# Performance work log

Measured on AMD Instinct MI355X. Metric: run time of the kernel, lower is better.

Reference implementation:

```python
import jax, jax.numpy as jnp
import numpy as np

B, C, HH, WW = 256, 1024, 7, 7
S = HH * WW            # 49 tokens
D = 1024               # hidden_size
L = 2                  # encoder_layers (nhead arg, swapped in source)
H = 2                  # attention heads (num_layers arg, swapped in source)
HD = D // H            # 512 head dim
FF = 1024              # encoder_ffn_dim
OUT = 1024             # head output
EPS = 1e-5


def setup_inputs() -> dict:
    key = jax.random.key(0)
    ks = jax.random.split(key, 10)
    n = lambda k, shape: jax.random.normal(k, shape, jnp.float32) * 0.02
    return dict(
        x=jax.random.normal(ks[0], (B, C, HH, WW), jnp.float32),
        pos_emb=n(ks[1], (S, D)),
        ln1_s=jnp.ones((L, D), jnp.float32), ln1_b=jnp.zeros((L, D), jnp.float32),
        wq=n(ks[2], (L, D, D)), wk=n(ks[3], (L, D, D)),
        wv=n(ks[4], (L, D, D)), wo=n(ks[5], (L, D, D)),
        ln2_s=jnp.ones((L, D), jnp.float32), ln2_b=jnp.zeros((L, D), jnp.float32),
        w1=n(ks[6], (L, D, FF)), b1=jnp.zeros((L, FF), jnp.float32),
        w2=n(ks[7], (L, FF, D)), b2=jnp.zeros((L, D), jnp.float32),
        lnf_s=jnp.ones((D,), jnp.float32), lnf_b=jnp.zeros((D,), jnp.float32),
        head_w=n(ks[8], (S * D, OUT)), head_b=jnp.zeros((OUT,), jnp.float32),
    )


def _ln(x, s, b):
    m = jnp.mean(x, axis=-1, keepdims=True)
    v = jnp.var(x, axis=-1, keepdims=True)
    return (x - m) * jax.lax.rsqrt(v + EPS) * s + b


def reference(x, pos_emb, ln1_s, ln1_b, wq, wk, wv, wo, ln2_s, ln2_b,
              w1, b1, w2, b2, lnf_s, lnf_b, head_w, head_b):
    b = x.shape[0]
    # flatten HxW then permute -> [B, S, D] token sequence
    h = x.reshape(b, C, S).transpose(0, 2, 1)
    # BigBirdPegasus encoder: learned pos emb added to inputs_embeds (no scaling path)
    h = h + pos_emb[None, :, :]
    scale = 1.0 / jnp.sqrt(jnp.float32(HD))
    for i in range(L):
        # --- self-attention block (pre-LN); seq_len=49 triggers original_full attention ---
        r = h
        hn = _ln(h, ln1_s[i], ln1_b[i])
        q = (hn @ wq[i]).reshape(b, S, H, HD)
        k = (hn @ wk[i]).reshape(b, S, H, HD)
        v = (hn @ wv[i]).reshape(b, S, H, HD)
        scores = jnp.einsum('bqhd,bkhd->bhqk', q, k) * scale
        attn = jax.nn.softmax(scores, axis=-1)
        ctx = jnp.einsum('bhqk,bkhd->bqhd', attn, v).reshape(b, S, D)
        h = r + ctx @ wo[i]
        # --- feed-forward block (pre-LN, gelu_new) ---
        r = h
        hn = _ln(h, ln2_s[i], ln2_b[i])
        hn = jax.nn.gelu(hn @ w1[i] + b1[i], approximate=True)
        h = r + hn @ w2[i] + b2[i]
    # BigBirdPegasus applies layernorm_embedding AFTER the layer stack
    h = _ln(h, lnf_s, lnf_b)
    # flatten + linear + relu head
    out = jax.nn.relu(h.reshape(b, S * D) @ head_w + head_b)
    return out
```

## Files before the change

kernel.cpp:

```cpp
#include <hip/hip_runtime.h>
#include <hip/hip_bf16.h>
#include <stdint.h>

#define Bq 256
#define Sq 49
#define Dq 1024
#define Hq 2
#define HDq 512
#define Mq (Bq*Sq)
#define KHEADq (Sq*Dq)
#define STq 3072

typedef unsigned short u16;
typedef short bf16x8 __attribute__((ext_vector_type(8)));
typedef float f32x4 __attribute__((ext_vector_type(4)));

__device__ inline u16 f2bf(float f){
  union { float f; uint32_t u; } c; c.f = f;
  uint32_t r = c.u + 0x7FFFu + ((c.u >> 16) & 1u);
  return (u16)(r >> 16);
}

#define GLOAD_LDS16(gp, lp) \
  __builtin_amdgcn_global_load_lds((__attribute__((address_space(1))) void*)(gp), \
                                   (__attribute__((address_space(3))) void*)(lp), 16, 0, 0)
#define MFMA16(a,b,c) __builtin_amdgcn_mfma_f32_16x16x32_bf16(a,b,c,0,0,0)

__global__ __launch_bounds__(256) void prep_kernel(const float* __restrict__ x,
    const float* __restrict__ pos, float* __restrict__ h){
  __shared__ float t[49*129];
  int b = blockIdx.x, c0 = blockIdx.y*128;
  int tid = threadIdx.x, lane = tid & 63, wave = tid >> 6;
  const float* xb = x + (size_t)b*(Dq*Sq) + (size_t)c0*Sq;
  #pragma unroll
  for(int i=0;i<32;i++){
    int cc = wave + i*4;
    if(lane < Sq) t[lane*129 + cc] = xb[(size_t)cc*Sq + lane];
  }
  __syncthreads();
  #pragma unroll
  for(int p=0;p<25;p++){
    int idx = p*256 + tid;
    int s = idx >> 7, cc = idx & 127;
    if(s < Sq)
      h[((size_t)b*Sq + s)*Dq + c0 + cc] = t[s*129 + cc] + pos[s*Dq + c0 + cc];
  }
}

__global__ __launch_bounds__(256) void ln_kernel(const float* __restrict__ hin,
    const float* __restrict__ sc, const float* __restrict__ bi, u16* __restrict__ outp){
  int wave = threadIdx.x >> 6, lane = threadIdx.x & 63;
  int row = blockIdx.x*4 + wave;
  const float* p = hin + (size_t)row*Dq + lane*16;
  float v[16];
  #pragma unroll
  for(int i=0;i<4;i++){
    f32x4 t = *(const f32x4*)(p + i*4);
    v[4*i]=t[0]; v[4*i+1]=t[1]; v[4*i+2]=t[2]; v[4*i+3]=t[3];
  }
  float s=0.f, sq=0.f;
  #pragma unroll
  for(int i=0;i<16;i++){ s += v[i]; sq += v[i]*v[i]; }
  #pragma unroll
  for(int o=32;o>=1;o>>=1){ s += __shfl_xor(s,o); sq += __shfl_xor(sq,o); }
  float mean = s * (1.f/Dq);
  float var  = sq * (1.f/Dq) - mean*mean;
  float rs = rsqrtf(var + 1e-5f);
  int c0 = lane*16;
  uint32_t w[8];
  #pragma unroll
  for(int i=0;i<8;i++){
    u16 lo = f2bf((v[2*i]   - mean)*rs*sc[c0+2*i]   + bi[c0+2*i]);
    u16 hi = f2bf((v[2*i+1] - mean)*rs*sc[c0+2*i+1] + bi[c0+2*i+1]);
    w[i] = (uint32_t)lo | ((uint32_t)hi << 16);
  }
  uint4* ob = (uint4*)(outp + (size_t)row*Dq + c0);
  ob[0] = make_uint4(w[0],w[1],w[2],w[3]);
  ob[1] = make_uint4(w[4],w[5],w[6],w[7]);
}

__global__ void transp_all(const float* __restrict__ wq, const float* __restrict__ wk,
    const float* __restrict__ wv, const float* __restrict__ wo,
    const float* __restrict__ w1, const float* __restrict__ w2, u16* __restrict__ outp){
  __shared__ float t[32][33];
  int slot = blockIdx.z; int l = slot / 6, j = slot - l*6;
  const float* srcs[6] = {wq,wk,wv,wo,w1,w2};
  const float* in = srcs[j] + (size_t)l*Dq*Dq;
  u16* o = outp + (size_t)slot*Dq*Dq;
  int k0 = blockIdx.x*32, n0 = blockIdx.y*32;
  int tx = threadIdx.x, ty = threadIdx.y;
  #pragma unroll
  for(int i=0;i<4;i++) t[ty+8*i][tx] = in[(size_t)(k0+ty+8*i)*Dq + n0+tx];
  __syncthreads();
  #pragma unroll
  for(int i=0;i<4;i++) o[(size_t)(n0+ty+8*i)*Dq + k0+tx] = f2bf(t[tx][ty+8*i]);
}

template<int EPI>
__global__ __launch_bounds__(512, 2) void gemm_nt2(
    const u16* __restrict__ A, int lda,
    const u16* __restrict__ Bt, int ldb,
    void* __restrict__ Cout, const float* __restrict__ resid,
    const float* __restrict__ bias, int ldc)
{
  __shared__ u16 lds[65536];
  int tid = threadIdx.x, lane = tid & 63;
  int wave = tid >> 6;
  int wm = wave >> 2, wn = wave & 3;
  int l15 = lane & 15, l4 = lane >> 4;
  int swz = (l15 & 7) << 4;

  int gx = gridDim.x, nwg = gx*gridDim.y;
  int orig = blockIdx.y*gx + blockIdx.x;
  int qq = nwg >> 3, rr = nwg & 7;
  int xcd = orig & 7, idx = orig >> 3;
  int wgid = (xcd < rr ? xcd*(qq+1) : rr*(qq+1) + (xcd-rr)*qq) + idx;
  int bx = wgid % gx, by = wgid / gx;
  int m0 = by*256, n0 = bx*256;

  int srow = tid >> 3, scolb = (tid & 7) * 16;
  int scolx = scolb ^ ((srow & 7) << 4);
  auto stage2 = [&](int d, int kt, int h){
    #pragma unroll
    for(int cc=0; cc<2; cc++){
      int c = 2*h + cc;
      if(c < 4){
        int row = c*64 + srow;
        const u16* src = A + (size_t)(m0+row)*lda + kt*64 + (scolx>>1);
        GLOAD_LDS16(src, &lds[d*16384 + c*4096 + tid*8]);
      } else {
        int c4 = c - 4;
        int row = c4*64 + srow;
        const u16* src = Bt + (size_t)(n0+row)*ldb + kt*64 + (scolx>>1);
        GLOAD_LDS16(src, &lds[32768 + d*16384 + c4*4096 + tid*8]);
      }
    }
  };
  auto rdA = [&](int d, int i, int s)->bf16x8{
    int row = wm*128 + i*16 + l15;
    int byt = row*128 + ((s*64 + l4*16) ^ swz);
    return *(const bf16x8*)((const char*)lds + d*32768 + byt);
  };
  auto rdB = [&](int d, int n, int s)->bf16x8{
    int row = wn*64 + n*16 + l15;
    int byt = row*128 + ((s*64 + l4*16) ^ swz);
    return *(const bf16x8*)((const char*)lds + 65536 + d*32768 + byt);
  };

  f32x4 acc[8][4] = {};
  bf16x8 bfr[4][2];

  #pragma unroll
  for(int h=0;h<4;h++) stage2(0, 0, h);

  for(int t=0; t<16; ++t){
    int d = t & 1;
    if(t+1 < 16){
      stage2(d^1, t+1, 0);
      asm volatile("s_waitcnt vmcnt(2)" ::: "memory");
    } else {
      asm volatile("s_waitcnt vmcnt(0)" ::: "memory");
    }
    __builtin_amdgcn_sched_barrier(0);
    __builtin_amdgcn_s_barrier();
    #pragma unroll
    for(int n=0;n<4;n++)
      #pragma unroll
      for(int s=0;s<2;s++)
        bfr[n][s] = rdB(d, n, s);
    {
      bf16x8 a00 = rdA(d,0,0), a01 = rdA(d,0,1), a10 = rdA(d,1,0), a11 = rdA(d,1,1);
      __builtin_amdgcn_s_setprio(1);
      #pragma unroll
      for(int n=0;n<4;n++){
        acc[0][n] = MFMA16(a00, bfr[n][0], acc[0][n]);
        acc[0][n] = MFMA16(a01, bfr[n][1], acc[0][n]);
        acc[1][n] = MFMA16(a10, bfr[n][0], acc[1][n]);
        acc[1][n] = MFMA16(a11, bfr[n][1], acc[1][n]);
      }
      __builtin_amdgcn_s_setprio(0);
      __builtin_amdgcn_s_barrier();
    }
    #pragma unroll
    for(int q=1;q<4;q++){
      bf16x8 a00 = rdA(d,2*q,0), a01 = rdA(d,2*q,1), a10 = rdA(d,2*q+1,0), a11 = rdA(d,2*q+1,1);
      if(t+1 < 16) stage2(d^1, t+1, q);
      __builtin_amdgcn_s_barrier();
      __builtin_amdgcn_s_setprio(1);
      #pragma unroll
      for(int n=0;n<4;n++){
        acc[2*q][n]   = MFMA16(a00, bfr[n][0], acc[2*q][n]);
        acc[2*q][n]   = MFMA16(a01, bfr[n][1], acc[2*q][n]);
        acc[2*q+1][n] = MFMA16(a10, bfr[n][0], acc[2*q+1][n]);
        acc[2*q+1][n] = MFMA16(a11, bfr[n][1], acc[2*q+1][n]);
      }
      __builtin_amdgcn_s_setprio(0);
      __builtin_amdgcn_s_barrier();
    }
  }

  if constexpr (EPI == 1){
    float* slot = (float*)((char*)lds + wave*4096);
    float bv[4];
    #pragma unroll
    for(int n=0;n<4;n++) bv[n] = bias ? bias[n0 + wn*64 + n*16 + l15] : 0.f;
    #pragma unroll
    for(int i=0;i<8;i++){
      #pragma unroll
      for(int n=0;n<4;n++)
        #pragma unroll
        for(int r=0;r<4;r++)
          slot[(l4*4+r)*64 + n*16 + l15] = acc[i][n][r] + bv[n];
      #pragma unroll
      for(int st=0;st<4;st++){
        int u = st*64 + lane;
        int row = u >> 4, c4 = (u & 15)*4;
        f32x4 v4 = *(const f32x4*)&slot[row*64 + c4];
        size_t o = (size_t)(m0 + wm*128 + i*16 + row)*ldc + n0 + wn*64 + c4;
        f32x4 r4 = *(const f32x4*)&resid[o];
        *(f32x4*)((float*)Cout + o) = v4 + r4;
      }
    }
  } else {
    u16* slot = (u16*)((char*)lds + wave*2048);
    float bv[4];
    if constexpr (EPI == 2){
      #pragma unroll
      for(int n=0;n<4;n++) bv[n] = bias[n0 + wn*64 + n*16 + l15];
    }
    #pragma unroll
    for(int i=0;i<8;i++){
      #pragma unroll
      for(int n=0;n<4;n++)
        #pragma unroll
        for(int r=0;r<4;r++){
          float va = acc[i][n][r];
          u16 ov;
          if constexpr (EPI == 0){
            ov = f2bf(va);
          } else {
            float xg = va + bv[n];
            float tg = tanhf(0.79788456080286536f*(xg + 0.044715f*xg*xg*xg));
            ov = f2bf(0.5f*xg*(1.f+tg));
          }
          slot[(l4*4+r)*64 + n*16 + l15] = ov;
        }
      #pragma unroll
      for(int st=0;st<2;st++){
        int u = st*64 + lane;
        int row = u >> 3, c8 = (u & 7)*8;
        bf16x8 v8 = *(const bf16x8*)&slot[row*64 + c8];
        *(bf16x8*)((u16*)Cout + (size_t)(m0 + wm*128 + i*16 + row)*ldc + n0 + wn*64 + c8) = v8;
      }
    }
  }
}

__global__ __launch_bounds__(256) void gemm_head(
    const u16* __restrict__ A, const float* __restrict__ W,
    float* __restrict__ parts)
{
  __shared__ u16 sA[128*32];
  __shared__ float sC[4][1024];
  int tid = threadIdx.x, lane = tid & 63;
  int wave = tid >> 6;
  int wm = wave >> 1, wn = wave & 1;
  int l15 = lane & 15, l4 = lane >> 4;
  int nwg = gridDim.x*gridDim.y*gridDim.z;
  int orig = (blockIdx.z*gridDim.y + blockIdx.y)*gridDim.x + blockIdx.x;
  int cpx = nwg >> 3;
  int swz = (orig & 7)*cpx + (orig >> 3);
  int bx = swz & 7, by = (swz >> 3) & 1, z = swz >> 4;
  int m0 = by*128, n0 = bx*128;
  size_t abase = (size_t)m0*KHEADq + (size_t)z*1024;
  f32x4 acc[4][4] = {};
  const float* wp = W + ((size_t)z*1024 + (size_t)l4*8)*1024 + n0 + wn*64 + l15;
  for(int kt=0;kt<32;kt++){
    #pragma unroll
    for(int c=0;c<2;c++){
      int s2 = c*256+tid;
      GLOAD_LDS16(A + abase + (size_t)(s2>>2)*KHEADq + kt*32 + (s2&3)*8, &sA[s2*8]);
    }
    float wreg[4][8];
    #pragma unroll
    for(int f=0;f<4;f++)
      #pragma unroll
      for(int jj=0;jj<8;jj++)
        wreg[f][jj] = wp[(size_t)(kt*32+jj)*1024 + f*16];
    bf16x8 bfr[4];
    #pragma unroll
    for(int f=0;f<4;f++){
      bf16x8 bv;
      #pragma unroll
      for(int jj=0;jj<8;jj++)
        bv[jj] = __builtin_bit_cast(short, __float2bfloat16(wreg[f][jj]));
      bfr[f] = bv;
    }
    __syncthreads();
    bf16x8 af[4];
    #pragma unroll
    for(int f=0;f<4;f++)
      af[f] = *(const bf16x8*)&sA[(wm*64 + f*16 + l15)*32 + l4*8];
    #pragma unroll
    for(int i=0;i<4;i++)
      #pragma unroll
      for(int j=0;j<4;j++)
        acc[i][j] = MFMA16(af[i], bfr[j], acc[i][j]);
    __syncthreads();
  }
  float* base = parts + (size_t)z*(Bq*1024);
  #pragma unroll
  for(int i=0;i<4;i++){
    #pragma unroll
    for(int j=0;j<4;j++)
      #pragma unroll
      for(int r=0;r<4;r++)
        sC[wave][(l4*4+r)*64 + j*16 + l15] = acc[i][j][r];
    #pragma unroll
    for(int st=0;st<4;st++){
      int u = st*64 + lane;
      int row = u >> 4, c4 = (u & 15)*4;
      f32x4 v4 = *(const f32x4*)&sC[wave][row*64 + c4];
      *(f32x4*)(base + (size_t)(m0+wm*64+i*16+row)*1024 + n0+wn*64+c4) = v4;
    }
  }
}

__global__ __launch_bounds__(256) void attn_kernel(u16* __restrict__ qkv)
{
  __shared__ float sS[64][65];
  __shared__ u16 sP[64][64];
  int bh = blockIdx.x;
  int b = bh >> 1, h = bh & 1;
  int tid = threadIdx.x, lane = tid & 63, wave = tid >> 6;
  int l15 = lane & 15, l4 = lane >> 4;
  f32x4 zero4 = {0.f,0.f,0.f,0.f};
  bf16x8 zb = {0,0,0,0,0,0,0,0};
  f32x4 acc[4];
  #pragma unroll
  for(int i=0;i<4;i++) acc[i] = zero4;
  int srow = wave*16 + l15;
  const u16* qp = qkv + (size_t)(b*Sq + srow)*STq + h*HDq + l4*8;
  const u16* kbase = qkv + (size_t)b*Sq*STq + Dq + h*HDq + l4*8;
  for(int kt=0;kt<16;kt++){
    bf16x8 aq = (srow < Sq) ? *(const bf16x8*)(qp + kt*32) : zb;
    #pragma unroll
    for(int fn=0;fn<4;fn++){
      int s2 = fn*16 + l15;
      bf16x8 bk = (s2 < Sq) ? *(const bf16x8*)(kbase + (size_t)s2*STq + kt*32) : zb;
      acc[fn] = MFMA16(aq, bk, acc[fn]);
    }
  }
  const float scale = 0.04419417382415922f;
  #pragma unroll
  for(int fn=0;fn<4;fn++)
    #pragma unroll
    for(int r=0;r<4;r++)
      sS[wave*16 + l4*4 + r][fn*16 + l15] = acc[fn][r]*scale;
  __syncthreads();
  if(tid < 64){
    float mx = -1e30f;
    for(int j=0;j<Sq;j++) mx = fmaxf(mx, sS[tid][j]);
    float sum = 0.f;
    for(int j=0;j<Sq;j++){ float e = __expf(sS[tid][j]-mx); sS[tid][j]=e; sum+=e; }
    float inv = 1.f/sum;
    for(int j=0;j<64;j++) sP[tid][j] = (j<Sq)? f2bf(sS[tid][j]*inv) : (u16)0;
  }
  __syncthreads();
  bf16x8 ap[2];
  #pragma unroll
  for(int kt2=0;kt2<2;kt2++)
    ap[kt2] = *(const bf16x8*)&sP[wave*16 + l15][kt2*32 + l4*8];
  const u16* vbp = qkv + (size_t)b*Sq*STq + 2*Dq + h*HDq + l15;
  u16* cb = qkv + (size_t)b*Sq*STq + h*HDq;
  for(int fn=0;fn<32;fn++){
    f32x4 c4 = zero4;
    #pragma unroll
    for(int kt2=0;kt2<2;kt2++){
      const u16* vp = vbp + fn*16 + (size_t)(kt2*32 + l4*8)*STq;
      bf16x8 bv;
      #pragma unroll
      for(int jj=0;jj<8;jj++) bv[jj] = (short)vp[(size_t)jj*STq];
      c4 = MFMA16(ap[kt2], bv, c4);
    }
    #pragma unroll
    for(int r=0;r<4;r++){
      int s = wave*16 + l4*4 + r;
      if(s < Sq) cb[(size_t)s*STq + fn*16 + l15] = f2bf(c4[r]);
    }
  }
}

__global__ __launch_bounds__(256) void head_finalize(const float* __restrict__ parts,
    const float* __restrict__ hb, float* __restrict__ outp){
  int idx = blockIdx.x*256 + threadIdx.x;
  float s = hb[idx & 1023];
  #pragma unroll
  for(int z=0;z<49;z++) s += parts[(size_t)z*(Bq*1024) + idx];
  outp[idx] = fmaxf(s, 0.f);
}

extern "C" void kernel_launch(void* const* d_in, const int* in_sizes, int n_in,
                              void* d_out, int out_size, void* d_ws, size_t ws_size,
                              hipStream_t stream) {
  (void)in_sizes; (void)n_in; (void)out_size;
  const float* x    = (const float*)d_in[0];
  const float* pos  = (const float*)d_in[1];
  const float* ln1s = (const float*)d_in[2];
  const float* ln1b = (const float*)d_in[3];
  const float* wq   = (const float*)d_in[4];
  const float* wk   = (const float*)d_in[5];
  const float* wv   = (const float*)d_in[6];
  const float* wo   = (const float*)d_in[7];
  const float* ln2s = (const float*)d_in[8];
  const float* ln2b = (const float*)d_in[9];
  const float* w1   = (const float*)d_in[10];
  const float* b1   = (const float*)d_in[11];
  const float* w2   = (const float*)d_in[12];
  const float* b2   = (const float*)d_in[13];
  const float* lnfs = (const float*)d_in[14];
  const float* lnfb = (const float*)d_in[15];
  const float* hw   = (const float*)d_in[16];
  const float* hb   = (const float*)d_in[17];
  float* out = (float*)d_out;

  char* ws = (char*)d_ws;
  size_t off = 0;
  auto carve = [&](size_t n) -> char* { char* p = ws + off; off += (n + 255) & ~(size_t)255; return p; };
  float* h    = (float*)carve((size_t)Mq*Dq*4);
  u16*  act0  = (u16*) carve((size_t)Mq*Dq*2);
  u16*  act1  = (u16*) carve((size_t)Mq*Dq*2);
  u16*  qkv   = (u16*) carve((size_t)(Mq+16)*STq*2);
  u16*  wT    = (u16*) carve((size_t)12*Dq*Dq*2);
  float* parts= (float*)qkv;
  if (off > ws_size) return;

  hipMemsetAsync(qkv + (size_t)Mq*STq, 0, (size_t)16*STq*2, stream);

  prep_kernel<<<dim3(Bq, 8), 256, 0, stream>>>(x, pos, h);
  transp_all<<<dim3(32,32,12), dim3(32,8), 0, stream>>>(wq, wk, wv, wo, w1, w2, wT);

  dim3 gg(4, Mq/256);
  dim3 gq(12, Mq/256);
  for(int l=0;l<2;l++){
    u16* qkvT = wT + (size_t)(l*6+0)*Dq*Dq;
    u16* woT  = wT + (size_t)(l*6+3)*Dq*Dq;
    u16* w1T  = wT + (size_t)(l*6+4)*Dq*Dq;
    u16* w2T  = wT + (size_t)(l*6+5)*Dq*Dq;

    ln_kernel<<<Mq/4, 256, 0, stream>>>(h, ln1s + l*Dq, ln1b + l*Dq, act0);
    gemm_nt2<0><<<gq, 512, 0, stream>>>(act0, Dq, qkvT, Dq, qkv, nullptr, nullptr, STq);
    attn_kernel<<<Bq*Hq, 256, 0, stream>>>(qkv);
    gemm_nt2<1><<<gg, 512, 0, stream>>>(qkv, STq, woT, Dq, h, h, nullptr, Dq);
    ln_kernel<<<Mq/4, 256, 0, stream>>>(h, ln2s + l*Dq, ln2b + l*Dq, act0);
    gemm_nt2<2><<<gg, 512, 0, stream>>>(act0, Dq, w1T, Dq, act1, nullptr, b1 + l*Dq, Dq);
    gemm_nt2<1><<<gg, 512, 0, stream>>>(act1, Dq, w2T, Dq, h, h, b2 + l*Dq, Dq);
  }

  ln_kernel<<<Mq/4, 256, 0, stream>>>(h, lnfs, lnfb, act0);
  gemm_head<<<dim3(8,2,49), 256, 0, stream>>>(act0, hw, parts);
  head_finalize<<<1024, 256, 0, stream>>>(parts, hb, out);
}
```

Measured before the change: 738.1 us.

## Store residual stream in bf16 and reorder GEMM B-fragment loads

The residual stream h moves from fp32 to bf16 storage. The prep kernel, layernorm loads and the residual-add GEMM epilogue now read and write bf16, which halves traffic on those tensors. The GEMM main loop is also restructured: B fragments load in two halves, and the first prefetch stage overlaps with the first MFMA block, to shorten LDS read stalls. Rounding the residual to bf16 after every layer adds accumulated precision error. Other kernels not shown, such as the final layernorm and head, must still agree with the new bf16 type.

```diff
diff --git a/kernel.cpp b/kernel.cpp
--- a/kernel.cpp
+++ b/kernel.cpp
@@ -20,6 +20,10 @@
   uint32_t r = c.u + 0x7FFFu + ((c.u >> 16) & 1u);
   return (u16)(r >> 16);
 }
+__device__ inline float bf2f(u16 h){
+  union { uint32_t u; float f; } c; c.u = ((uint32_t)h) << 16;
+  return c.f;
+}
 
 #define GLOAD_LDS16(gp, lp) \
   __builtin_amdgcn_global_load_lds((__attribute__((address_space(1))) void*)(gp), \
@@ -27,7 +31,7 @@
 #define MFMA16(a,b,c) __builtin_amdgcn_mfma_f32_16x16x32_bf16(a,b,c,0,0,0)
 
 __global__ __launch_bounds__(256) void prep_kernel(const float* __restrict__ x,
-    const float* __restrict__ pos, float* __restrict__ h){
+    const float* __restrict__ pos, u16* __restrict__ h){
   __shared__ float t[49*129];
   int b = blockIdx.x, c0 = blockIdx.y*128;
   int tid = threadIdx.x, lane = tid & 63, wave = tid >> 6;
@@ -43,20 +47,25 @@
     int idx = p*256 + tid;
     int s = idx >> 7, cc = idx & 127;
     if(s < Sq)
-      h[((size_t)b*Sq + s)*Dq + c0 + cc] = t[s*129 + cc] + pos[s*Dq + c0 + cc];
-  }
-}
-
-__global__ __launch_bounds__(256) void ln_kernel(const float* __restrict__ hin,
+      h[((size_t)b*Sq + s)*Dq + c0 + cc] = f2bf(t[s*129 + cc] + pos[s*Dq + c0 + cc]);
+  }
+}
+
+__global__ __launch_bounds__(256) void ln_kernel(const u16* __restrict__ hin,
     const float* __restrict__ sc, const float* __restrict__ bi, u16* __restrict__ outp){
   int wave = threadIdx.x >> 6, lane = threadIdx.x & 63;
   int row = blockIdx.x*4 + wave;
-  const float* p = hin + (size_t)row*Dq + lane*16;
+  const u16* p = hin + (size_t)row*Dq + lane*16;
+  uint4 t0 = *(const uint4*)p;
+  uint4 t1 = *(const uint4*)(p + 8);
   float v[16];
-  #pragma unroll
-  for(int i=0;i<4;i++){
-    f32x4 t = *(const f32x4*)(p + i*4);
-    v[4*i]=t[0]; v[4*i+1]=t[1]; v[4*i+2]=t[2]; v[4*i+3]=t[3];
+  {
+    uint32_t wds[8] = {t0.x,t0.y,t0.z,t0.w,t1.x,t1.y,t1.z,t1.w};
+    #pragma unroll
+    for(int i=0;i<8;i++){
+      v[2*i]   = bf2f((u16)(wds[i] & 0xffff));
+      v[2*i+1] = bf2f((u16)(wds[i] >> 16));
+    }
   }
   float s=0.f, sq=0.f;
   #pragma unroll
@@ -100,7 +109,7 @@
 __global__ __launch_bounds__(512, 2) void gemm_nt2(
     const u16* __restrict__ A, int lda,
     const u16* __restrict__ Bt, int ldb,
-    void* __restrict__ Cout, const float* __restrict__ resid,
+    void* __restrict__ Cout, const u16* __restrict__ resid,
     const float* __restrict__ bias, int ldc)
 {
   __shared__ u16 lds[65536];
@@ -148,14 +157,14 @@
   };
 
   f32x4 acc[8][4] = {};
-  bf16x8 bfr[4][2];
 
   #pragma unroll
   for(int h=0;h<4;h++) stage2(0, 0, h);
 
   for(int t=0; t<16; ++t){
     int d = t & 1;
-    if(t+1 < 16){
+    bf16x8 bfr[4][2];
+    if(t < 15){
       stage2(d^1, t+1, 0);
       asm volatile("s_waitcnt vmcnt(2)" ::: "memory");
     } else {
@@ -163,44 +172,47 @@
     }
     __builtin_amdgcn_sched_barrier(0);
     __builtin_amdgcn_s_barrier();
-    #pragma unroll
-    for(int n=0;n<4;n++)
-      #pragma unroll
-      for(int s=0;s<2;s++)
-        bfr[n][s] = rdB(d, n, s);
-    {
-      bf16x8 a00 = rdA(d,0,0), a01 = rdA(d,0,1), a10 = rdA(d,1,0), a11 = rdA(d,1,1);
+    bfr[0][0]=rdB(d,0,0); bfr[0][1]=rdB(d,0,1);
+    bfr[1][0]=rdB(d,1,0); bfr[1][1]=rdB(d,1,1);
+    bf16x8 a0s0=rdA(d,0,0), a0s1=rdA(d,0,1), a1s0=rdA(d,1,0), a1s1=rdA(d,1,1);
+    __builtin_amdgcn_s_setprio(1);
+    acc[0][0]=MFMA16(a0s0,bfr[0][0],acc[0][0]); acc[0][0]=MFMA16(a0s1,bfr[0][1],acc[0][0]);
+    acc[0][1]=MFMA16(a0s0,bfr[1][0],acc[0][1]); acc[0][1]=MFMA16(a0s1,bfr[1][1],acc[0][1]);
+    acc[1][0]=MFMA16(a1s0,bfr[0][0],acc[1][0]); acc[1][0]=MFMA16(a1s1,bfr[0][1],acc[1][0]);
+    acc[1][1]=MFMA16(a1s0,bfr[1][0],acc[1][1]); acc[1][1]=MFMA16(a1s1,bfr[1][1],acc[1][1]);
+    __builtin_amdgcn_s_setprio(0);
+    __builtin_amdgcn_s_barrier();
+    bfr[2][0]=rdB(d,2,0); bfr[2][1]=rdB(d,2,1);
+    bfr[3][0]=rdB(d,3,0); bfr[3][1]=rdB(d,3,1);
+    if(t < 15) stage2(d^1, t+1, 1);
+    __builtin_amdgcn_s_barrier();
+    __builtin_amdgcn_s_setprio(1);
+    acc[0][2]=MFMA16(a0s0,bfr[2][0],acc[0][2]); acc[0][2]=MFMA16(a0s1,bfr[2][1],acc[0][2]);
+    acc[0][3]=MFMA16(a0s0,bfr[3][0],acc[0][3]); acc[0][3]=MFMA16(a0s1,bfr[3][1],acc[0][3]);
+    acc[1][2]=MFMA16(a1s0,bfr[2][0],acc[1][2]); acc[1][2]=MFMA16(a1s1,bfr[2][1],acc[1][2]);
+    acc[1][3]=MFMA16(a1s0,bfr[3][0],acc[1][3]); acc[1][3]=MFMA16(a1s1,bfr[3][1],acc[1][3]);
+    __builtin_amdgcn_s_setprio(0);
+    __builtin_amdgcn_s_barrier();
+    #pragma unroll
+    for(int q=1;q<4;q++){
+      bf16x8 c0s0=rdA(d,2*q,0), c0s1=rdA(d,2*q,1), c1s0=rdA(d,2*q+1,0), c1s1=rdA(d,2*q+1,1);
+      if(t < 15 && q < 3) stage2(d^1, t+1, q+1);
+      __builtin_amdgcn_s_barrier();
       __builtin_amdgcn_s_setprio(1);
       #pragma unroll
       for(int n=0;n<4;n++){
-        acc[0][n] = MFMA16(a00, bfr[n][0], acc[0][n]);
-        acc[0][n] = MFMA16(a01, bfr[n][1], acc[0][n]);
-        acc[1][n] = MFMA16(a10, bfr[n][0], acc[1][n]);
-        acc[1][n] = MFMA16(a11, bfr[n][1], acc[1][n]);
+        acc[2*q][n]   = MFMA16(c0s0, bfr[n][0], acc[2*q][n]);
+        acc[2*q][n]   = MFMA16(c0s1, bfr[n][1], acc[2*q][n]);
+        acc[2*q+1][n] = MFMA16(c1s0, bfr[n][0], acc[2*q+1][n]);
+        acc[2*q+1][n] = MFMA16(c1s1, bfr[n][1], acc[2*q+1][n]);
       }
       __builtin_amdgcn_s_setprio(0);
       __builtin_amdgcn_s_barrier();
     }
-    #pragma unroll
-    for(int q=1;q<4;q++){
-      bf16x8 a00 = rdA(d,2*q,0), a01 = rdA(d,2*q,1), a10 = rdA(d,2*q+1,0), a11 = rdA(d,2*q+1,1);
-      if(t+1 < 16) stage2(d^1, t+1, q);
-      __builtin_amdgcn_s_barrier();
-      __builtin_amdgcn_s_setprio(1);
-      #pragma unroll
-      for(int n=0;n<4;n++){
-        acc[2*q][n]   = MFMA16(a00, bfr[n][0], acc[2*q][n]);
-        acc[2*q][n]   = MFMA16(a01, bfr[n][1], acc[2*q][n]);
-        acc[2*q+1][n] = MFMA16(a10, bfr[n][0], acc[2*q+1][n]);
-        acc[2*q+1][n] = MFMA16(a11, bfr[n][1], acc[2*q+1][n]);
-      }
-      __builtin_amdgcn_s_setprio(0);
-      __builtin_amdgcn_s_barrier();
-    }
   }
 
   if constexpr (EPI == 1){
-    float* slot = (float*)((char*)lds + wave*4096);
+    float* slotf = (float*)((char*)lds + wave*4096);
     float bv[4];
     #pragma unroll
     for(int n=0;n<4;n++) bv[n] = bias ? bias[n0 + wn*64 + n*16 + l15] : 0.f;
@@ -210,15 +222,22 @@
       for(int n=0;n<4;n++)
         #pragma unroll
         for(int r=0;r<4;r++)
-          slot[(l4*4+r)*64 + n*16 + l15] = acc[i][n][r] + bv[n];
-      #pragma unroll
-      for(int st=0;st<4;st++){
+          slotf[(l4*4+r)*64 + n*16 + l15] = acc[i][n][r] + bv[n];
+      #pragma unroll
+      for(int st=0;st<2;st++){
         int u = st*64 + lane;
-        int row = u >> 4, c4 = (u & 15)*4;
-        f32x4 v4 = *(const f32x4*)&slot[row*64 + c4];
-        size_t o = (size_t)(m0 + wm*128 + i*16 + row)*ldc + n0 + wn*64 + c4;
-        f32x4 r4 = *(const f32x4*)&resid[o];
-        *(f32x4*)((float*)Cout + o) = v4 + r4;
+        int row = u >> 3, c8 = (u & 7)*8;
+        f32x4 lo = *(const f32x4*)&slotf[row*64 + c8];
+        f32x4 hi = *(const f32x4*)&slotf[row*64 + c8 + 4];
+        size_t o = (size_t)(m0 + wm*128 + i*16 + row)*ldc + n0 + wn*64 + c8;
+        bf16x8 rb = *(const bf16x8*)(resid + o);
+        bf16x8 ov;
+        #pragma unroll
+        for(int j=0;j<4;j++){
+          ov[j]   = (short)f2bf(lo[j] + bf2f((u16)rb[j]));
+          ov[4+j] = (short)f2bf(hi[j] + bf2f((u16)rb[4+j]));
+        }
+        *(bf16x8*)((u16*)Cout + o) = ov;
       }
     }
   } else {
@@ -427,7 +446,7 @@
   char* ws = (char*)d_ws;
   size_t off = 0;
   auto carve = [&](size_t n) -> char* { char* p = ws + off; off += (n + 255) & ~(size_t)255; return p; };
-  float* h    = (float*)carve((size_t)Mq*Dq*4);
+  u16*  h     = (u16*) carve((size_t)Mq*Dq*2);
   u16*  act0  = (u16*) carve((size_t)Mq*Dq*2);
   u16*  act1  = (u16*) carve((size_t)Mq*Dq*2);
   u16*  qkv   = (u16*) carve((size_t)(Mq+16)*STq*2);
```

After: 683.6 us. 1.08x faster.
